# Optimization experiments

Measured on AMD Instinct MI355X. Metric: run time of the kernel, lower is better.

Reference implementation:

```python
import jax, jax.numpy as jnp
import numpy as np

B, SQ, SK, D = 8, 2048, 768, 768  # SK must equal D for layer_combine concat to typecheck


def setup_inputs() -> dict:
    key = jax.random.key(0)
    ks = jax.random.split(key, 13)
    s = 0.02
    return {
        "query": jax.random.normal(ks[0], (B, SQ, D), jnp.float32),
        "key_matrix": jax.random.normal(ks[1], (B, SK, D), jnp.float32),
        "value_matrix": jax.random.normal(ks[2], (B, SK, D), jnp.float32),
        "prev_layer": jax.random.normal(ks[3], (SK, D), jnp.float32) * s,
        "attention_mask": jax.random.randint(ks[4], (B, 1, SK), 0, 2, jnp.int32),
        "Wq": jax.random.normal(ks[5], (D, D), jnp.float32) * s,
        "bq": jax.random.normal(ks[6], (D,), jnp.float32) * s,
        "Wk": jax.random.normal(ks[7], (D, D), jnp.float32) * s,
        "bk": jax.random.normal(ks[8], (D,), jnp.float32) * s,
        "Wv": jax.random.normal(ks[9], (D, D), jnp.float32) * s,
        "bv": jax.random.normal(ks[10], (D,), jnp.float32) * s,
        "Wc": jax.random.normal(ks[11], (D, 2 * D), jnp.float32) * s,
        "bc": jax.random.normal(ks[12], (D,), jnp.float32) * s,
    }


def reference(query, key_matrix, value_matrix, prev_layer, attention_mask,
              Wq, bq, Wk, bk, Wv, bv, Wc, bc):
    # Linear projections (torch Linear: x @ W.T + b)
    Q = query @ Wq.T + bq                      # [B, SQ, D]
    K = key_matrix @ Wk.T + bk                 # [B, SK, D]
    V = value_matrix @ Wv.T + bv               # computed but unused when prev_layer given (faithful)
    scale = 1.0 / np.sqrt(D).astype(np.float32)
    scores = jnp.einsum('bqd,bkd->bqk', Q, K) * scale  # [B, SQ, SK]
    scores = jnp.where(attention_mask == 0, jnp.float32(-1e9), scores)
    # prev-layer integration: matmul + concat + linear combine
    layer_attn = scores @ prev_layer           # [B, SQ, D]
    combined = jnp.concatenate([scores, layer_attn], axis=-1)  # [B, SQ, 2D]
    out = combined @ Wc.T + bc                 # [B, SQ, D]
    return out
```

## Files before the change

kernel.cpp:

```cpp
#include <hip/hip_runtime.h>
#include <hip/hip_bf16.h>


typedef __attribute__((ext_vector_type(8))) short short8;
typedef __attribute__((ext_vector_type(4))) float f32x4;
typedef __attribute__((ext_vector_type(4))) unsigned int u32x4;

#define SCALE 0.03608439182435161f

__device__ inline unsigned short f2bf(float x) {
  unsigned int u = __builtin_bit_cast(unsigned int, x);
  u = (u + 0x7fffu + ((u >> 16) & 1u)) >> 16;
  return (unsigned short)u;
}
__device__ inline float bf2f(unsigned short h) {
  return __builtin_bit_cast(float, ((unsigned int)h) << 16);
}
__device__ inline unsigned int pack_trunc(float hi, float lo) {
  return __builtin_amdgcn_perm(__builtin_bit_cast(unsigned int, hi),
                               __builtin_bit_cast(unsigned int, lo), 0x07060302u);
}

__global__ void k_prep(const float* __restrict__ prev, const float* __restrict__ Wc,
                       unsigned short* __restrict__ prev_bf,
                       unsigned short* __restrict__ Wc2_bf) {
  int g = blockIdx.x;
  int region = g / 576;
  int idx = (g - region * 576) * 256 + threadIdx.x;
  float4 v;
  unsigned short* dst;
  if (region == 0) { v = reinterpret_cast<const float4*>(prev)[idx]; dst = prev_bf; }
  else {
    int r = idx / 192, c4 = (idx - r * 192) * 4;
    v = *reinterpret_cast<const float4*>(Wc + (long long)r * 1536 + 768 + c4);
    dst = Wc2_bf;
  }
  reinterpret_cast<ushort4*>(dst)[idx] = make_ushort4(f2bf(v.x), f2bf(v.y), f2bf(v.z), f2bf(v.w));
}

__global__ void k_tposeW(const float* __restrict__ Wq, const float* __restrict__ Wk,
                         unsigned short* __restrict__ WqT, unsigned short* __restrict__ WkT) {
  __shared__ float t[64][65];
  const float* src = blockIdx.z ? Wk : Wq;
  unsigned short* dst = blockIdx.z ? WkT : WqT;
  int bx = blockIdx.x * 64, by = blockIdx.y * 64;
  int tx = threadIdx.x & 63, ty = threadIdx.x >> 6;
  #pragma unroll
  for (int i = 0; i < 64; i += 4)
    t[ty + i][tx] = src[(long long)(by + ty + i) * 768 + bx + tx];
  __syncthreads();
  #pragma unroll
  for (int i = 0; i < 64; i += 4)
    dst[(long long)(bx + ty + i) * 768 + by + tx] = f2bf(t[tx][ty + i]);
}

__global__ void k_cvtz(const float* __restrict__ key, const int* __restrict__ mask,
                       unsigned short* __restrict__ keyzT) {
  __shared__ float t[64][65];
  int b = blockIdx.z;
  const float* src = key + (long long)b * 589824;
  unsigned short* dst = keyzT + (long long)b * 589824;
  const int* mb = mask + b * 768;
  int bx = blockIdx.x * 64, by = blockIdx.y * 64;
  int tx = threadIdx.x & 63, ty = threadIdx.x >> 6;
  #pragma unroll
  for (int i = 0; i < 64; i += 4) {
    float v = src[(long long)(by + ty + i) * 768 + bx + tx];
    t[ty + i][tx] = mb[by + ty + i] ? v : 0.0f;
  }
  __syncthreads();
  #pragma unroll
  for (int i = 0; i < 64; i += 4)
    dst[(long long)(bx + ty + i) * 768 + by + tx] = f2bf(t[tx][ty + i]);
}

__global__ void k_scalars(const unsigned short* __restrict__ WqT,
                          const unsigned short* __restrict__ WkT,
                          const float* __restrict__ bk, const float* __restrict__ bq,
                          float* __restrict__ u, float* __restrict__ w3) {
  int gw = blockIdx.x * 4 + (threadIdx.x >> 6);
  int lane = threadIdx.x & 63;
  if (gw >= 1536) return;
  const unsigned short* wrow = (gw < 768) ? (WqT + (long long)gw * 768)
                                          : (WkT + (long long)(gw - 768) * 768);
  const float* vec = (gw < 768) ? bk : bq;
  float s = 0.f;
  for (int j = lane; j < 768; j += 64) s += bf2f(wrow[j]) * vec[j];
  #pragma unroll
  for (int off = 32; off > 0; off >>= 1) s += __shfl_down(s, off, 64);
  if (lane == 0) { if (gw < 768) u[gw] = s; else w3[gw - 768] = s; }
}

__global__ void k_scol(const float* __restrict__ Mt, const int* __restrict__ mask,
                       float* __restrict__ s1, float* __restrict__ sm0) {
  int gw = blockIdx.x * 4 + (threadIdx.x >> 6);
  int lane = threadIdx.x & 63;
  int b = gw / 768, d2 = gw - b * 768;
  if (b >= 8) return;
  const int* mb = mask + b * 768;
  const float* mrow = Mt + (long long)d2 * 768;
  float a1 = 0.f, a0 = 0.f;
  for (int k = lane; k < 768; k += 64) {
    float v = mrow[k];
    if (mb[k]) a1 += v; else a0 += v;
  }
  #pragma unroll
  for (int off = 32; off > 0; off >>= 1) {
    a1 += __shfl_down(a1, off, 64);
    a0 += __shfl_down(a0, off, 64);
  }
  if (lane == 0) { s1[gw] = a1; sm0[gw] = a0; }
}

__global__ void k_row(const unsigned short* __restrict__ Tt, const float* __restrict__ w3,
                      const float* __restrict__ s1, const float* __restrict__ sm0,
                      const float* __restrict__ bq, const float* __restrict__ bk,
                      const float* __restrict__ bc, float* __restrict__ row) {
  int gw = blockIdx.x * 4 + (threadIdx.x >> 6);
  int lane = threadIdx.x & 63;
  int b = gw / 768, d2 = gw - b * 768;
  if (b >= 8) return;
  const unsigned short* trow = Tt + ((long long)b * 768 + d2) * 768;
  float st = 0.f, sbb = 0.f;
  for (int j = lane; j < 768; j += 64) {
    st += bf2f(trow[j]) * w3[j];
    sbb += bq[j] * bk[j];
  }
  #pragma unroll
  for (int off = 32; off > 0; off >>= 1) {
    st += __shfl_down(st, off, 64);
    sbb += __shfl_down(sbb, off, 64);
  }
  if (lane == 0)
    row[gw] = bc[d2] - 1e9f * sm0[gw] + SCALE * (st + sbb * s1[gw]);
}

template <int MODE, int BM, int BN, int AF32>
__global__ __launch_bounds__(256) void gemm_nt(
    const void* __restrict__ A, long long aStr, int lda,
    const unsigned short* __restrict__ B, long long bStr, int ldb,
    float* __restrict__ Cf, unsigned short* __restrict__ Cbf,
    long long cStr, int ldc,
    const float* __restrict__ aux, const float* __restrict__ aux2)
{
  constexpr int BK = 64;
  constexpr int EA = AF32 ? 4 : 2;
  constexpr int AGR = BK * EA / 16;
  constexpr int MI = BM / 32, NJ = BN / 32;
  constexpr int AGT = BM * AGR / 256, BGT = BN * 8 / 256;
  constexpr int ARB = BK * EA;
  __shared__ __align__(16) char As[BM * BK * EA];
  __shared__ __align__(16) char Bs[BN * BK * 2];

  const int gx = gridDim.x, gy = gridDim.y;
  const int nwg = gx * gy * (int)gridDim.z;
  int lin = blockIdx.x + gx * (blockIdx.y + gy * blockIdx.z);
  int qq = nwg >> 3, rr = nwg & 7, xcd = lin & 7, loc = lin >> 3;
  int swz = (xcd < rr ? xcd * (qq + 1) : rr * (qq + 1) + (xcd - rr) * qq) + loc;
  int bz = swz / (gx * gy);
  int rem = swz - bz * gx * gy;
  int by = rem / gx, bx = rem - by * gx;

  const int b = bz;
  const char* Ab = (const char*)A + (long long)b * aStr * EA;
  const unsigned short* Bb = B + (long long)b * bStr;
  const int m0 = by * BM, n0 = bx * BN;

  const int tid = threadIdx.x;
  const int w = tid >> 6, lane = tid & 63;
  const int wr = w >> 1, wc = w & 1;
  const int fr = lane & 15, fq = lane >> 4;

  f32x4 acc[MI][NJ] = {};

  for (int kt = 0; kt < 768; kt += BK) {
    __syncthreads();
    #pragma unroll
    for (int t = 0; t < AGT; ++t) {
      int g = t * 256 + tid;
      int row = g / AGR, s = g & (AGR - 1);
      int sg = (s - row) & (AGR - 1);
      long long boff = ((long long)(m0 + row) * lda + kt) * EA + sg * 16;
      __builtin_amdgcn_global_load_lds(
          (const __attribute__((address_space(1))) void*)(Ab + boff),
          (__attribute__((address_space(3))) void*)(As + g * 16), 16, 0, 0);
    }
    #pragma unroll
    for (int t = 0; t < BGT; ++t) {
      int g = t * 256 + tid;
      int row = g >> 3, s = g & 7;
      int sg = (s - row) & 7;
      const unsigned short* gb = Bb + (long long)(n0 + row) * ldb + kt + sg * 8;
      __builtin_amdgcn_global_load_lds(
          (const __attribute__((address_space(1))) void*)gb,
          (__attribute__((address_space(3))) void*)(Bs + g * 16), 16, 0, 0);
    }
    __syncthreads();

    #pragma unroll
    for (int kk = 0; kk < 2; ++kk) {
      short8 af[MI], bfr[NJ];
      #pragma unroll
      for (int i = 0; i < MI; ++i) {
        int r = wr * (BM / 2) + i * 16 + fr;
        if constexpr (AF32) {
          const f32x4* base = (const f32x4*)(As + r * ARB);
          int gidx = kk * 8 + fq * 2;
          f32x4 x = base[(gidx + r) & 15];
          f32x4 y = base[(gidx + 1 + r) & 15];
          unsigned int p0 = pack_trunc(x[1], x[0]), p1 = pack_trunc(x[3], x[2]);
          unsigned int p2 = pack_trunc(y[1], y[0]), p3 = pack_trunc(y[3], y[2]);
          u32x4 u4 = {p0, p1, p2, p3};
          af[i] = __builtin_bit_cast(short8, u4);
        } else {
          int sgi = ((kk * 4 + fq) + r) & 7;
          af[i] = *reinterpret_cast<const short8*>(As + r * 128 + sgi * 16);
        }
      }
      #pragma unroll
      for (int j = 0; j < NJ; ++j) {
        int r = wc * (BN / 2) + j * 16 + fr;
        int sgj = ((kk * 4 + fq) + r) & 7;
        bfr[j] = *reinterpret_cast<const short8*>(Bs + r * 128 + sgj * 16);
      }
      #pragma unroll
      for (int i = 0; i < MI; ++i)
        #pragma unroll
        for (int j = 0; j < NJ; ++j)
          acc[i][j] = __builtin_amdgcn_mfma_f32_16x16x32_bf16(af[i], bfr[j], acc[i][j], 0, 0, 0);
    }
  }

  #pragma unroll
  for (int i = 0; i < MI; ++i)
    #pragma unroll
    for (int j = 0; j < NJ; ++j)
      #pragma unroll
      for (int r = 0; r < 4; ++r) {
        int row = m0 + wr * (BM / 2) + i * 16 + fq * 4 + r;
        int col = n0 + wc * (BN / 2) + j * 16 + fr;
        float v = acc[i][j][r];
        if constexpr (MODE == 0) {
          v += aux[(long long)row * 1536 + col];
          Cf[(long long)row * 768 + col] = v;
          Cbf[(long long)row * 768 + col] = f2bf(v);
        } else if constexpr (MODE == 2) {
          Cbf[(long long)b * cStr + (long long)row * ldc + col] = f2bf(v);
        } else if constexpr (MODE == 5) {
          v += aux[b * 768 + row] * aux2[col];
          Cbf[(long long)b * cStr + (long long)row * ldc + col] = f2bf(v);
        } else {
          Cf[(long long)b * cStr + (long long)row * ldc + col] = v * SCALE + aux[b * 768 + col];
        }
      }
}

extern "C" void kernel_launch(void* const* d_in, const int* in_sizes, int n_in,
                              void* d_out, int out_size, void* d_ws, size_t ws_size,
                              hipStream_t stream)
{
  const float* query = (const float*)d_in[0];
  const float* key   = (const float*)d_in[1];
  const float* prev  = (const float*)d_in[3];
  const int*   mask  = (const int*)d_in[4];
  const float* Wq    = (const float*)d_in[5];
  const float* bq    = (const float*)d_in[6];
  const float* Wk    = (const float*)d_in[7];
  const float* bk    = (const float*)d_in[8];
  const float* Wc    = (const float*)d_in[11];
  const float* bc    = (const float*)d_in[12];
  float* out = (float*)d_out;

  char* p = (char*)d_ws;
  size_t off = 0;
  auto alloc = [&](size_t bytes) {
    char* r = p + off;
    off += (bytes + 255) & ~(size_t)255;
    return r;
  };
  unsigned short* keyzT_bf = (unsigned short*)alloc(4718592ull * 2);
  unsigned short* WqT_bf   = (unsigned short*)alloc(589824ull * 2);
  unsigned short* WkT_bf   = (unsigned short*)alloc(589824ull * 2);
  unsigned short* prev_bf  = (unsigned short*)alloc(589824ull * 2);
  unsigned short* Wc2_bf   = (unsigned short*)alloc(589824ull * 2);
  float*          Mt_f     = (float*)alloc(589824ull * 4);
  unsigned short* Mt_bf    = (unsigned short*)alloc(589824ull * 2);
  unsigned short* W2_bf    = (unsigned short*)alloc(589824ull * 2);
  unsigned short* Tt_bf    = (unsigned short*)alloc(4718592ull * 2);
  unsigned short* Pt_bf    = (unsigned short*)alloc(4718592ull * 2);
  float*          s1f      = (float*)alloc(6144ull * 4);
  float*          sm0f     = (float*)alloc(6144ull * 4);
  float*          uv       = (float*)alloc(768ull * 4);
  float*          w3v      = (float*)alloc(768ull * 4);
  float*          rowv     = (float*)alloc(6144ull * 4);
  (void)ws_size; (void)in_sizes; (void)n_in; (void)out_size;

  k_tposeW<<<dim3(12, 12, 2), dim3(256), 0, stream>>>(Wq, Wk, WqT_bf, WkT_bf);
  k_prep<<<dim3(1152), dim3(256), 0, stream>>>(prev, Wc, prev_bf, Wc2_bf);
  k_cvtz<<<dim3(12, 12, 8), dim3(256), 0, stream>>>(key, mask, keyzT_bf);

  gemm_nt<0, 64, 64, 0><<<dim3(12, 12, 1), dim3(256), 0, stream>>>(
      (const void*)Wc2_bf, 0ll, 768, prev_bf, 0ll, 768, Mt_f, Mt_bf, 0ll, 768,
      Wc, (const float*)nullptr);
  gemm_nt<2, 64, 64, 0><<<dim3(12, 12, 1), dim3(256), 0, stream>>>(
      (const void*)WqT_bf, 0ll, 768, WkT_bf, 0ll, 768, (float*)nullptr, W2_bf, 0ll, 768,
      (const float*)nullptr, (const float*)nullptr);
  k_scalars<<<dim3(384), dim3(256), 0, stream>>>(WqT_bf, WkT_bf, bk, bq, uv, w3v);
  k_scol<<<dim3(1536), dim3(256), 0, stream>>>(Mt_f, mask, s1f, sm0f);
  gemm_nt<2, 64, 64, 0><<<dim3(12, 12, 8), dim3(256), 0, stream>>>(
      (const void*)Mt_bf, 0ll, 768, keyzT_bf, 589824ll, 768, (float*)nullptr, Tt_bf,
      589824ll, 768, (const float*)nullptr, (const float*)nullptr);
  gemm_nt<5, 64, 64, 0><<<dim3(12, 12, 8), dim3(256), 0, stream>>>(
      (const void*)Tt_bf, 589824ll, 768, W2_bf, 0ll, 768, (float*)nullptr, Pt_bf,
      589824ll, 768, s1f, uv);
  k_row<<<dim3(1536), dim3(256), 0, stream>>>(Tt_bf, w3v, s1f, sm0f, bq, bk, bc, rowv);
  gemm_nt<4, 128, 128, 1><<<dim3(6, 16, 8), dim3(256), 0, stream>>>(
      (const void*)query, 1572864ll, 768, Pt_bf, 589824ll, 768, out,
      (unsigned short*)nullptr, 1572864ll, 768, rowv, (const float*)nullptr);
}
```

Measured before the change: 123.4 us.

## Stage fp32 A tiles through registers with bf16 packing and prefetch

For the fp32-A GEMM variant, A tiles are now loaded into registers, packed to bf16, and written to LDS instead of being staged as fp32 through LDS via direct global-to-LDS loads. The next tile's A loads are issued before computing the current tile, overlapping global latency with MFMA work. This halves the A footprint in LDS and removes per-fragment packing from the inner loop, at the cost of more registers and a serial B load after compute.

```diff
diff --git a/kernel.cpp b/kernel.cpp
--- a/kernel.cpp
+++ b/kernel.cpp
@@ -135,7 +135,7 @@
     row[gw] = bc[d2] - 1e9f * sm0[gw] + SCALE * (st + sbb * s1[gw]);
 }
 
-template <int MODE, int BM, int BN, int AF32>
+template <int MODE, int BM, int BN, int AREG>
 __global__ __launch_bounds__(256) void gemm_nt(
     const void* __restrict__ A, long long aStr, int lda,
     const unsigned short* __restrict__ B, long long bStr, int ldb,
@@ -144,12 +144,9 @@
     const float* __restrict__ aux, const float* __restrict__ aux2)
 {
   constexpr int BK = 64;
-  constexpr int EA = AF32 ? 4 : 2;
-  constexpr int AGR = BK * EA / 16;
   constexpr int MI = BM / 32, NJ = BN / 32;
-  constexpr int AGT = BM * AGR / 256, BGT = BN * 8 / 256;
-  constexpr int ARB = BK * EA;
-  __shared__ __align__(16) char As[BM * BK * EA];
+  constexpr int AGT = BM * 8 / 256, BGT = BN * 8 / 256;
+  __shared__ __align__(16) char As[BM * BK * 2];
   __shared__ __align__(16) char Bs[BN * BK * 2];
 
   const int gx = gridDim.x, gy = gridDim.y;
@@ -162,9 +159,8 @@
   int by = rem / gx, bx = rem - by * gx;
 
   const int b = bz;
-  const char* Ab = (const char*)A + (long long)b * aStr * EA;
+  const int m0 = by * BM, n0 = bx * BN;
   const unsigned short* Bb = B + (long long)b * bStr;
-  const int m0 = by * BM, n0 = bx * BN;
 
   const int tid = threadIdx.x;
   const int w = tid >> 6, lane = tid & 63;
@@ -173,18 +169,41 @@
 
   f32x4 acc[MI][NJ] = {};
 
-  for (int kt = 0; kt < 768; kt += BK) {
-    __syncthreads();
+  const unsigned short* Ab16 = (const unsigned short*)A + (AREG ? 0 : (long long)b * aStr);
+  const float*          Abf  = (const float*)A + (AREG ? (long long)b * aStr : 0);
+  const int arow = tid >> 1, ahalf = tid & 1;
+  f32x4 areg[8];
+
+  auto loadA = [&](int kt) {
+    const float* src = Abf + (long long)(m0 + arow) * lda + kt + ahalf * 32;
+    #pragma unroll
+    for (int j = 0; j < 8; ++j)
+      areg[j] = *reinterpret_cast<const f32x4*>(src + j * 4);
+  };
+  auto packWriteA = [&]() {
+    #pragma unroll
+    for (int jj = 0; jj < 4; ++jj) {
+      f32x4 x = areg[2 * jj], y = areg[2 * jj + 1];
+      u32x4 u4 = {pack_trunc(x[1], x[0]), pack_trunc(x[3], x[2]),
+                  pack_trunc(y[1], y[0]), pack_trunc(y[3], y[2])};
+      int c = ahalf * 4 + jj;
+      int g = arow * 8 + ((c + arow) & 7);
+      *reinterpret_cast<short8*>(As + g * 16) = __builtin_bit_cast(short8, u4);
+    }
+  };
+  auto gloadA = [&](int kt) {
     #pragma unroll
     for (int t = 0; t < AGT; ++t) {
       int g = t * 256 + tid;
-      int row = g / AGR, s = g & (AGR - 1);
-      int sg = (s - row) & (AGR - 1);
-      long long boff = ((long long)(m0 + row) * lda + kt) * EA + sg * 16;
+      int row = g >> 3, s = g & 7;
+      int sg = (s - row) & 7;
+      const unsigned short* ga = Ab16 + (long long)(m0 + row) * lda + kt + sg * 8;
       __builtin_amdgcn_global_load_lds(
-          (const __attribute__((address_space(1))) void*)(Ab + boff),
+          (const __attribute__((address_space(1))) void*)ga,
           (__attribute__((address_space(3))) void*)(As + g * 16), 16, 0, 0);
     }
+  };
+  auto gloadB = [&](int kt) {
     #pragma unroll
     for (int t = 0; t < BGT; ++t) {
       int g = t * 256 + tid;
@@ -195,27 +214,16 @@
           (const __attribute__((address_space(1))) void*)gb,
           (__attribute__((address_space(3))) void*)(Bs + g * 16), 16, 0, 0);
     }
-    __syncthreads();
-
+  };
+  auto compute = [&]() {
     #pragma unroll
     for (int kk = 0; kk < 2; ++kk) {
       short8 af[MI], bfr[NJ];
       #pragma unroll
       for (int i = 0; i < MI; ++i) {
         int r = wr * (BM / 2) + i * 16 + fr;
-        if constexpr (AF32) {
-          const f32x4* base = (const f32x4*)(As + r * ARB);
-          int gidx = kk * 8 + fq * 2;
-          f32x4 x = base[(gidx + r) & 15];
-          f32x4 y = base[(gidx + 1 + r) & 15];
-          unsigned int p0 = pack_trunc(x[1], x[0]), p1 = pack_trunc(x[3], x[2]);
-          unsigned int p2 = pack_trunc(y[1], y[0]), p3 = pack_trunc(y[3], y[2]);
-          u32x4 u4 = {p0, p1, p2, p3};
-          af[i] = __builtin_bit_cast(short8, u4);
-        } else {
-          int sgi = ((kk * 4 + fq) + r) & 7;
-          af[i] = *reinterpret_cast<const short8*>(As + r * 128 + sgi * 16);
-        }
+        int sgi = ((kk * 4 + fq) + r) & 7;
+        af[i] = *reinterpret_cast<const short8*>(As + r * 128 + sgi * 16);
       }
       #pragma unroll
       for (int j = 0; j < NJ; ++j) {
@@ -228,6 +236,31 @@
         #pragma unroll
         for (int j = 0; j < NJ; ++j)
           acc[i][j] = __builtin_amdgcn_mfma_f32_16x16x32_bf16(af[i], bfr[j], acc[i][j], 0, 0, 0);
+    }
+  };
+
+  if constexpr (AREG) {
+    gloadB(0);
+    loadA(0);
+    packWriteA();
+    __syncthreads();
+    for (int t = 0; t < 12; ++t) {
+      if (t < 11) loadA((t + 1) * BK);
+      compute();
+      __syncthreads();
+      if (t < 11) {
+        gloadB((t + 1) * BK);
+        packWriteA();
+        __syncthreads();
+      }
+    }
+  } else {
+    for (int kt = 0; kt < 768; kt += BK) {
+      __syncthreads();
+      gloadA(kt);
+      gloadB(kt);
+      __syncthreads();
+      compute();
     }
   }
 
```

After: 144.9 us. 1.17x slower.
